# Optimization experiments

Measured on AMD Instinct MI355X. Metric: run time of the kernel, lower is better.

## Reference

```python
import jax, jax.numpy as jnp
import numpy as np

N_NODES = 50000
N_EDGES = 800000
HIDDEN = 128
N_LAYERS = 3
N_MASKED = 25000
N_GRAPHS = 64


def setup_inputs() -> dict:
    key = jax.random.key(0)
    ks = jax.random.split(key, 8)
    scale = 1.0 / np.sqrt(HIDDEN)
    return {
        "x": jax.random.normal(ks[0], (N_NODES, HIDDEN), dtype=jnp.float32),
        "edge_index": jax.random.randint(ks[1], (2, N_EDGES), 0, N_NODES, dtype=jnp.int64),
        "mask": jax.random.randint(ks[2], (N_MASKED,), 0, N_NODES, dtype=jnp.int64),
        "batch": jnp.sort(jax.random.randint(ks[3], (N_MASKED,), 0, N_GRAPHS, dtype=jnp.int64)),
        "conv_w": jax.random.normal(ks[4], (N_LAYERS, HIDDEN, HIDDEN), dtype=jnp.float32) * scale,
        "conv_b": jnp.zeros((N_LAYERS, HIDDEN), dtype=jnp.float32),
        "lt1_w": jax.random.normal(ks[5], (HIDDEN,), dtype=jnp.float32) * scale,
        "lt1_b": jnp.zeros((1,), dtype=jnp.float32),
    }


def reference(x, edge_index, mask, batch, conv_w, conv_b, lt1_w, lt1_b):
    n = x.shape[0]
    # GCNConv: add self-loops, symmetric normalization D^-1/2 (A+I) D^-1/2
    loops = jnp.arange(n, dtype=edge_index.dtype)
    src = jnp.concatenate([edge_index[0], loops])
    dst = jnp.concatenate([edge_index[1], loops])
    deg = jax.ops.segment_sum(jnp.ones_like(src, dtype=x.dtype), dst, num_segments=n)
    dinv = jax.lax.rsqrt(deg)  # deg >= 1 because of self-loops
    norm = (dinv[src] * dinv[dst])[:, None]  # [E+N, 1]

    h = x
    for l in range(N_LAYERS):
        hw = h @ conv_w[l]                                  # [N, H]
        agg = jax.ops.segment_sum(hw[src] * norm, dst, num_segments=n)
        h = jax.nn.elu(agg + conv_b[l])                     # dropout is identity in eval mode

    xm = h[mask]                                            # [M, H] masked-node features
    pooled = jax.ops.segment_max(xm, batch, num_segments=N_GRAPHS)  # global_max_pool
    return pooled @ lt1_w[:, None] + lt1_b                  # [G, 1]
```

## Files before the change

### kernel.cpp

```cpp
#include <hip/hip_runtime.h>
#include <math.h>

#define N_NODES  50000
#define N_EDGES  800000
#define HIDDEN   128
#define N_LAYERS 3
#define N_MASKED 25000
#define N_GRAPHS 64

typedef __attribute__((ext_vector_type(8))) short bf16x8;
typedef __attribute__((ext_vector_type(4))) float f32x4;

__device__ __forceinline__ unsigned fmap(float f) {
    unsigned u = __float_as_uint(f);
    return (u & 0x80000000u) ? ~u : (u | 0x80000000u);
}
__device__ __forceinline__ float funmap(unsigned u) {
    return __uint_as_float((u & 0x80000000u) ? (u & 0x7FFFFFFFu) : ~u);
}

__device__ __forceinline__ unsigned pack_split(float x) {
    unsigned u = __float_as_uint(x);
    unsigned hi = (u + 0x7fffu + ((u >> 16) & 1u)) >> 16;
    float rem = x - __uint_as_float(hi << 16);
    unsigned v = __float_as_uint(rem);
    unsigned lo = (v + 0x7fffu + ((v >> 16) & 1u)) >> 16;
    return hi | (lo << 16);
}

__global__ void count_deg_kernel(const int* __restrict__ dst, unsigned* __restrict__ deg) {
    int i = blockIdx.x * blockDim.x + threadIdx.x;
    if (i < N_EDGES) atomicAdd(&deg[dst[i]], 1u);
}

__global__ void dinv_kernel(const unsigned* __restrict__ deg, float* __restrict__ dinv) {
    int i = blockIdx.x * blockDim.x + threadIdx.x;
    if (i < N_NODES) dinv[i] = rsqrtf((float)(deg[i] + 1u));
}

__global__ void scan_block_kernel(const unsigned* __restrict__ deg, unsigned* __restrict__ incl,
                                  unsigned* __restrict__ bsum) {
    __shared__ unsigned s[1024];
    int i = blockIdx.x * 1024 + threadIdx.x;
    unsigned v = (i < N_NODES) ? deg[i] : 0u;
    s[threadIdx.x] = v;
    __syncthreads();
    for (int off = 1; off < 1024; off <<= 1) {
        unsigned t = (threadIdx.x >= off) ? s[threadIdx.x - off] : 0u;
        __syncthreads();
        s[threadIdx.x] += t;
        __syncthreads();
    }
    if (i < N_NODES) incl[i] = s[threadIdx.x];
    if (threadIdx.x == 1023) bsum[blockIdx.x] = s[1023];
}

__global__ void scan_bsum_kernel(unsigned* __restrict__ bsum, int n) {
    if (blockIdx.x == 0 && threadIdx.x == 0) {
        unsigned run = 0;
        for (int i = 0; i < n; ++i) { unsigned t = bsum[i]; bsum[i] = run; run += t; }
    }
}

__global__ void scan_finalize_kernel(const unsigned* __restrict__ incl,
                                     const unsigned* __restrict__ bsum_ex,
                                     unsigned* __restrict__ row_ptr,
                                     unsigned* __restrict__ cursor) {
    int i = blockIdx.x * blockDim.x + threadIdx.x;
    if (i <= N_NODES) {
        unsigned v = (i == 0) ? 0u : incl[i - 1] + bsum_ex[(i - 1) >> 10];
        row_ptr[i] = v;
        if (i < N_NODES) cursor[i] = v;
    }
}

__global__ void fill_csr_kernel(const int* __restrict__ src, const int* __restrict__ dst,
                                unsigned* __restrict__ cursor, int* __restrict__ csr_src) {
    int e = blockIdx.x * blockDim.x + threadIdx.x;
    if (e < N_EDGES) {
        unsigned p = atomicAdd(&cursor[dst[e]], 1u);
        csr_src[p] = src[e];
    }
}

__global__ void wprep_kernel(const float* __restrict__ W,
                             unsigned short* __restrict__ Whi,
                             unsigned short* __restrict__ Wlo) {
    int idx = blockIdx.x * 256 + threadIdx.x;
    if (idx >= 3 * 16384) return;
    int j     = idx & 7;
    int lane  = (idx >> 3) & 63;
    int ct    = (idx >> 9) & 7;
    int ks    = (idx >> 12) & 3;
    int layer = idx >> 14;
    int k = ks * 32 + (lane >> 4) * 8 + j;
    int n = ct * 16 + (lane & 15);
    unsigned p = pack_split(W[layer * 16384 + k * 128 + n]);
    Whi[idx] = (unsigned short)(p & 0xffffu);
    Wlo[idx] = (unsigned short)(p >> 16);
}

__global__ void xpack_kernel(const float* __restrict__ x, unsigned* __restrict__ xp, int n) {
    int i = blockIdx.x * 256 + threadIdx.x;
    if (i < n) xp[i] = pack_split(x[i]);
}

template<int MODE>
__global__ __launch_bounds__(256, 2) void mfma_gemm_kernel(const unsigned* __restrict__ Ap,
                                                           const unsigned short* __restrict__ Wh,
                                                           const unsigned short* __restrict__ Wl,
                                                           const float* __restrict__ dinv,
                                                           const float* __restrict__ bias,
                                                           const int* __restrict__ batch,
                                                           unsigned* __restrict__ gmax,
                                                           float* __restrict__ Out,
                                                           int nrows) {
    __shared__ __align__(16) unsigned short WhL[16384];
    __shared__ __align__(16) unsigned short WlL[16384];
    const int tid = threadIdx.x;
    const int lane = tid & 63;
    const int wv = tid >> 6;
    const int rowBase = blockIdx.x * 64 + wv * 16;
    const bool active = rowBase < nrows;

    int arow = rowBase + (lane & 15);
    if (arow > nrows - 1) arow = nrows - 1;
    const unsigned* aptr = Ap + (size_t)arow * 128 + (lane >> 4) * 8;
    uint4 pa[8];
    #pragma unroll
    for (int q = 0; q < 8; ++q)
        pa[q] = active ? *(const uint4*)(aptr + (q >> 1) * 32 + (q & 1) * 4)
                       : make_uint4(0, 0, 0, 0);

    {
        const uint4* gh = (const uint4*)Wh;
        const uint4* gl = (const uint4*)Wl;
        uint4* sh = (uint4*)WhL;
        uint4* sl = (uint4*)WlL;
        #pragma unroll
        for (int i = 0; i < 8; ++i) {
            sh[tid + i * 256] = gh[tid + i * 256];
            sl[tid + i * 256] = gl[tid + i * 256];
        }
    }
    __syncthreads();
    if (!active) return;

    f32x4 acc[8];
    #pragma unroll
    for (int c = 0; c < 8; ++c) acc[c] = (f32x4){0.f, 0.f, 0.f, 0.f};

    #pragma unroll
    for (int ks = 0; ks < 4; ++ks) {
        unsigned pv[8] = {pa[2*ks].x, pa[2*ks].y, pa[2*ks].z, pa[2*ks].w,
                          pa[2*ks+1].x, pa[2*ks+1].y, pa[2*ks+1].z, pa[2*ks+1].w};
        bf16x8 ah, al;
        #pragma unroll
        for (int j = 0; j < 8; ++j) {
            ah[j] = (short)(pv[j] & 0xffffu);
            al[j] = (short)(pv[j] >> 16);
        }
        const unsigned short* wbh = WhL + ks * 4096 + lane * 8;
        const unsigned short* wbl = WlL + ks * 4096 + lane * 8;
        #pragma unroll
        for (int ct = 0; ct < 8; ++ct) {
            bf16x8 bh = *(const bf16x8*)(wbh + ct * 512);
            bf16x8 bl = *(const bf16x8*)(wbl + ct * 512);
            acc[ct] = __builtin_amdgcn_mfma_f32_16x16x32_bf16(ah, bh, acc[ct], 0, 0, 0);
            acc[ct] = __builtin_amdgcn_mfma_f32_16x16x32_bf16(al, bh, acc[ct], 0, 0, 0);
            acc[ct] = __builtin_amdgcn_mfma_f32_16x16x32_bf16(ah, bl, acc[ct], 0, 0, 0);
        }
    }

    const int colBase = lane & 15;
    const int rgrp = lane >> 4;
    #pragma unroll
    for (int r = 0; r < 4; ++r) {
        int row = rowBase + rgrp * 4 + r;
        if (row >= nrows) continue;
        float d = 0.f;
        int bofs = 0;
        if (MODE == 0 || MODE == 1) d = dinv[row];
        if (MODE == 2) bofs = batch[row] * 128;
        #pragma unroll
        for (int ct = 0; ct < 8; ++ct) {
            int col = ct * 16 + colBase;
            float o = acc[ct][r];
            if (MODE == 0) {
                Out[(size_t)row * 128 + col] = o * d;
            } else {
                o += bias[col];
                o = o > 0.f ? o : expm1f(o);
                if (MODE == 1) Out[(size_t)row * 128 + col] = o * d;
                else           atomicMax(&gmax[bofs + col], fmap(o));
            }
        }
    }
}

template<int GMODE>
__global__ __launch_bounds__(256) void gather_kernel(const float* __restrict__ tab,
                                                     const unsigned* __restrict__ row_ptr,
                                                     const int* __restrict__ csr_src,
                                                     const float* __restrict__ dinv,
                                                     const float* __restrict__ bias,
                                                     float* __restrict__ outf,
                                                     unsigned* __restrict__ outp,
                                                     const int* __restrict__ nodes,
                                                     int n_items) {
    int wid = (blockIdx.x * blockDim.x + threadIdx.x) >> 6;
    int w = wid >> 1;
    if (w >= n_items) return;
    const int f = ((wid & 1) << 6) | (threadIdx.x & 63);
    const int v = nodes ? nodes[w] : w;

    const unsigned s0 = row_ptr[v], e0 = row_ptr[v + 1];
    const float* __restrict__ base = tab + f;

    float acc[8];
    #pragma unroll
    for (int j = 0; j < 8; ++j) acc[j] = 0.f;
    acc[0] = base[(size_t)v << 7];

    unsigned i = s0;
    if (i + 8 <= e0) {
        int idx[8];
        #pragma unroll
        for (int j = 0; j < 8; ++j) idx[j] = csr_src[i + j];
        for (; i + 16 <= e0; i += 8) {
            int nxt[8];
            #pragma unroll
            for (int j = 0; j < 8; ++j) nxt[j] = csr_src[i + 8 + j];
            #pragma unroll
            for (int j = 0; j < 8; ++j) acc[j] += base[(size_t)idx[j] << 7];
            #pragma unroll
            for (int j = 0; j < 8; ++j) idx[j] = nxt[j];
        }
        #pragma unroll
        for (int j = 0; j < 8; ++j) acc[j] += base[(size_t)idx[j] << 7];
        i += 8;
    }
    if (i + 4 <= e0) {
        #pragma unroll
        for (int j = 0; j < 4; ++j) acc[j] += base[(size_t)csr_src[i + j] << 7];
        i += 4;
    }
    for (; i < e0; ++i) acc[0] += base[(size_t)csr_src[i] << 7];

    float dv = dinv[v];
    float sumall = ((acc[0] + acc[1]) + (acc[2] + acc[3])) +
                   ((acc[4] + acc[5]) + (acc[6] + acc[7]));
    if (GMODE == 0) {
        float o = dv * sumall + bias[f];
        o = o > 0.f ? o : expm1f(o);
        outf[((size_t)w << 7) + f] = o * dv;
    } else {
        outp[((size_t)w << 7) + f] = pack_split(dv * sumall);
    }
}

__global__ void gmax_init_kernel(unsigned* __restrict__ gmax) {
    int i = blockIdx.x * blockDim.x + threadIdx.x;
    if (i < N_GRAPHS * 128) gmax[i] = 0x007FFFFFu;
}

__global__ void pool_finish_kernel(const unsigned* __restrict__ gmax,
                                   const float* __restrict__ w, const float* __restrict__ b,
                                   float* __restrict__ out) {
    const int g = blockIdx.x;
    const int f = threadIdx.x;
    float val = funmap(gmax[g * 128 + f]) * w[f];
    #pragma unroll
    for (int off = 32; off > 0; off >>= 1) val += __shfl_down(val, off);
    __shared__ float ps[2];
    if ((threadIdx.x & 63) == 0) ps[threadIdx.x >> 6] = val;
    __syncthreads();
    if (threadIdx.x == 0) out[g] = ps[0] + ps[1] + b[0];
}

extern "C" void kernel_launch(void* const* d_in, const int* in_sizes, int n_in,
                              void* d_out, int out_size, void* d_ws, size_t ws_size,
                              hipStream_t stream) {
    const float* x      = (const float*)d_in[0];
    const int*   ei     = (const int*)d_in[1];
    const int*   mask   = (const int*)d_in[2];
    const int*   batch  = (const int*)d_in[3];
    const float* conv_w = (const float*)d_in[4];
    const float* conv_b = (const float*)d_in[5];
    const float* lt1_w  = (const float*)d_in[6];
    const float* lt1_b  = (const float*)d_in[7];
    float* out = (float*)d_out;

    const int* e_src = ei;
    const int* e_dst = ei + N_EDGES;

    char* ws = (char*)d_ws;
    auto carve = [&](size_t bytes) { char* p = ws; ws += (bytes + 255) & ~(size_t)255; return p; };
    unsigned* deg     = (unsigned*)carve(N_NODES * 4);
    float*    dinv    = (float*)   carve(N_NODES * 4);
    unsigned* row_ptr = (unsigned*)carve((N_NODES + 1) * 4);
    unsigned* cursor  = (unsigned*)carve(N_NODES * 4);
    unsigned* bsum    = (unsigned*)carve(64 * 4);
    unsigned* gmax    = (unsigned*)carve(N_GRAPHS * 128 * 4);
    unsigned short* wph = (unsigned short*)carve(3 * 16384 * 2);
    unsigned short* wpl = (unsigned short*)carve(3 * 16384 * 2);
    int*      csr_src = (int*)     carve((size_t)N_EDGES * 4);
    char*     reg1    = carve((size_t)N_NODES * HIDDEN * 4);
    char*     reg2    = carve((size_t)N_NODES * HIDDEN * 4);
    unsigned* incl    = (unsigned*)csr_src;

    unsigned* xp    = (unsigned*)reg1;
    float*    bufB  = (float*)reg1;
    float*    bufB2 = (float*)reg1;
    float*    bufA  = (float*)reg2;
    unsigned* bufAp = (unsigned*)reg2;
    unsigned* bufCp = (unsigned*)reg2;

    const int NB_SCAN = (N_NODES + 1023) / 1024;

    hipMemsetAsync(deg, 0, N_NODES * sizeof(unsigned), stream);
    count_deg_kernel<<<(N_EDGES + 255) / 256, 256, 0, stream>>>(e_dst, deg);
    dinv_kernel<<<(N_NODES + 255) / 256, 256, 0, stream>>>(deg, dinv);
    scan_block_kernel<<<NB_SCAN, 1024, 0, stream>>>(deg, incl, bsum);
    scan_bsum_kernel<<<1, 64, 0, stream>>>(bsum, NB_SCAN);
    scan_finalize_kernel<<<(N_NODES + 256) / 256, 256, 0, stream>>>(incl, bsum, row_ptr, cursor);
    fill_csr_kernel<<<(N_EDGES + 255) / 256, 256, 0, stream>>>(e_src, e_dst, cursor, csr_src);
    gmax_init_kernel<<<(N_GRAPHS * 128 + 255) / 256, 256, 0, stream>>>(gmax);
    wprep_kernel<<<(3 * 16384 + 255) / 256, 256, 0, stream>>>(conv_w, wph, wpl);
    xpack_kernel<<<(N_NODES * HIDDEN + 255) / 256, 256, 0, stream>>>(x, xp, N_NODES * HIDDEN);

    const int GEMM_FULL = (N_NODES + 63) / 64;
    const int GEMM_MASK = (N_MASKED + 63) / 64;
    const int GA_FULL = (N_NODES * 2 * 64 + 255) / 256;
    const int GA_MASK = (N_MASKED * 2 * 64 + 255) / 256;

    mfma_gemm_kernel<0><<<GEMM_FULL, 256, 0, stream>>>(xp, wph, wpl, dinv, nullptr,
                                                       nullptr, nullptr, bufA, N_NODES);
    gather_kernel<0><<<GA_FULL, 256, 0, stream>>>(bufA, row_ptr, csr_src, dinv,
                                                  conv_b, bufB, nullptr, nullptr, N_NODES);
    gather_kernel<1><<<GA_FULL, 256, 0, stream>>>(bufB, row_ptr, csr_src, dinv,
                                                  nullptr, nullptr, bufAp, nullptr, N_NODES);
    mfma_gemm_kernel<1><<<GEMM_FULL, 256, 0, stream>>>(bufAp, wph + 16384, wpl + 16384, dinv,
                                                       conv_b + HIDDEN, nullptr, nullptr,
                                                       bufB2, N_NODES);
    gather_kernel<1><<<GA_MASK, 256, 0, stream>>>(bufB2, row_ptr, csr_src, dinv,
                                                  nullptr, nullptr, bufCp, mask, N_MASKED);
    mfma_gemm_kernel<2><<<GEMM_MASK, 256, 0, stream>>>(bufCp, wph + 32768, wpl + 32768, nullptr,
                                                       conv_b + 2 * HIDDEN, batch, gmax,
                                                       nullptr, N_MASKED);

    pool_finish_kernel<<<N_GRAPHS, HIDDEN, 0, stream>>>(gmax, lt1_w, lt1_b, out);
}
```

Before: 396.7 us.

## Store feature tables as 16-column slices and gather slice-wise with float4 lanes

The GEMM outputs and the layer-1 gather output now use a sliced layout: 8 slices of 16 columns, each slice stored contiguously for all nodes. The gather kernel assigns each block one slice and four nodes. Within a wave, 16 edges are processed in parallel with float4 loads of 64 bytes per row, and the partial sums are combined with shuffles. The goal is to keep each slice's working set (about 3.2 MB) resident in cache and to spread edge loads across lanes for more memory parallelism. In exchange, slice blocks repeat the index reads and row_ptr loads 8 times, and every gather ends with a shuffle reduction.

New measurement: 552.6 us. 39.3% more time.

```diff
diff --git a/kernel.cpp b/kernel.cpp
--- a/kernel.cpp
+++ b/kernel.cpp
@@ -7,6 +7,7 @@
 #define N_LAYERS 3
 #define N_MASKED 25000
 #define N_GRAPHS 64
+#define SLICE_STRIDE ((size_t)N_NODES * 16)
 
 typedef __attribute__((ext_vector_type(8))) short bf16x8;
 typedef __attribute__((ext_vector_type(4))) float f32x4;
@@ -113,7 +114,7 @@
                                                            const float* __restrict__ bias,
                                                            const int* __restrict__ batch,
                                                            unsigned* __restrict__ gmax,
-                                                           float* __restrict__ Out,
+                                                           float* __restrict__ OutS,
                                                            int nrows) {
     __shared__ __align__(16) unsigned short WhL[16384];
     __shared__ __align__(16) unsigned short WlL[16384];
@@ -187,75 +188,81 @@
             int col = ct * 16 + colBase;
             float o = acc[ct][r];
             if (MODE == 0) {
-                Out[(size_t)row * 128 + col] = o * d;
+                OutS[(size_t)ct * SLICE_STRIDE + (size_t)row * 16 + colBase] = o * d;
             } else {
                 o += bias[col];
                 o = o > 0.f ? o : expm1f(o);
-                if (MODE == 1) Out[(size_t)row * 128 + col] = o * d;
-                else           atomicMax(&gmax[bofs + col], fmap(o));
+                if (MODE == 1)
+                    OutS[(size_t)ct * SLICE_STRIDE + (size_t)row * 16 + colBase] = o * d;
+                else
+                    atomicMax(&gmax[bofs + col], fmap(o));
             }
         }
     }
 }
 
 template<int GMODE>
-__global__ __launch_bounds__(256) void gather_kernel(const float* __restrict__ tab,
+__global__ __launch_bounds__(256) void gather_kernel(const float* __restrict__ tabS,
                                                      const unsigned* __restrict__ row_ptr,
                                                      const int* __restrict__ csr_src,
                                                      const float* __restrict__ dinv,
                                                      const float* __restrict__ bias,
-                                                     float* __restrict__ outf,
+                                                     float* __restrict__ outS,
                                                      unsigned* __restrict__ outp,
                                                      const int* __restrict__ nodes,
                                                      int n_items) {
-    int wid = (blockIdx.x * blockDim.x + threadIdx.x) >> 6;
-    int w = wid >> 1;
+    const int b = blockIdx.x;
+    const int s = b & 7;
+    const int w = (b >> 3) * 4 + (threadIdx.x >> 6);
     if (w >= n_items) return;
-    const int f = ((wid & 1) << 6) | (threadIdx.x & 63);
+    const int lane = threadIdx.x & 63;
+    const int eq = lane >> 2;
+    const int q  = lane & 3;
     const int v = nodes ? nodes[w] : w;
 
+    const float4* __restrict__ tab4 = (const float4*)(tabS + (size_t)s * SLICE_STRIDE);
+
     const unsigned s0 = row_ptr[v], e0 = row_ptr[v + 1];
-    const float* __restrict__ base = tab + f;
-
-    float acc[8];
-    #pragma unroll
-    for (int j = 0; j < 8; ++j) acc[j] = 0.f;
-    acc[0] = base[(size_t)v << 7];
-
-    unsigned i = s0;
-    if (i + 8 <= e0) {
-        int idx[8];
-        #pragma unroll
-        for (int j = 0; j < 8; ++j) idx[j] = csr_src[i + j];
-        for (; i + 16 <= e0; i += 8) {
-            int nxt[8];
-            #pragma unroll
-            for (int j = 0; j < 8; ++j) nxt[j] = csr_src[i + 8 + j];
-            #pragma unroll
-            for (int j = 0; j < 8; ++j) acc[j] += base[(size_t)idx[j] << 7];
-            #pragma unroll
-            for (int j = 0; j < 8; ++j) idx[j] = nxt[j];
-        }
-        #pragma unroll
-        for (int j = 0; j < 8; ++j) acc[j] += base[(size_t)idx[j] << 7];
-        i += 8;
-    }
-    if (i + 4 <= e0) {
-        #pragma unroll
-        for (int j = 0; j < 4; ++j) acc[j] += base[(size_t)csr_src[i + j] << 7];
-        i += 4;
-    }
-    for (; i < e0; ++i) acc[0] += base[(size_t)csr_src[i] << 7];
-
-    float dv = dinv[v];
-    float sumall = ((acc[0] + acc[1]) + (acc[2] + acc[3])) +
-                   ((acc[4] + acc[5]) + (acc[6] + acc[7]));
-    if (GMODE == 0) {
-        float o = dv * sumall + bias[f];
-        o = o > 0.f ? o : expm1f(o);
-        outf[((size_t)w << 7) + f] = o * dv;
-    } else {
-        outp[((size_t)w << 7) + f] = pack_split(dv * sumall);
+    const int cnt = (int)(e0 - s0);
+
+    float4 a = make_float4(0.f, 0.f, 0.f, 0.f);
+    if (eq == 0) a = tab4[(size_t)v * 4 + q];
+
+    for (int i = 0; i < cnt; i += 16) {
+        int e = i + eq;
+        if (e < cnt) {
+            int src = csr_src[s0 + e];
+            float4 t = tab4[(size_t)src * 4 + q];
+            a.x += t.x; a.y += t.y; a.z += t.z; a.w += t.w;
+        }
+    }
+
+    #pragma unroll
+    for (int off = 32; off >= 4; off >>= 1) {
+        a.x += __shfl_down(a.x, off);
+        a.y += __shfl_down(a.y, off);
+        a.z += __shfl_down(a.z, off);
+        a.w += __shfl_down(a.w, off);
+    }
+
+    if (lane < 4) {
+        float dv = dinv[v];
+        if (GMODE == 0) {
+            float4 bb = *(const float4*)&bias[s * 16 + lane * 4];
+            float4 o;
+            o.x = dv * a.x + bb.x; o.y = dv * a.y + bb.y;
+            o.z = dv * a.z + bb.z; o.w = dv * a.w + bb.w;
+            o.x = o.x > 0.f ? o.x : expm1f(o.x);
+            o.y = o.y > 0.f ? o.y : expm1f(o.y);
+            o.z = o.z > 0.f ? o.z : expm1f(o.z);
+            o.w = o.w > 0.f ? o.w : expm1f(o.w);
+            o.x *= dv; o.y *= dv; o.z *= dv; o.w *= dv;
+            ((float4*)(outS + (size_t)s * SLICE_STRIDE + (size_t)w * 16))[lane] = o;
+        } else {
+            uint4 pk = make_uint4(pack_split(dv * a.x), pack_split(dv * a.y),
+                                  pack_split(dv * a.z), pack_split(dv * a.w));
+            ((uint4*)(outp + (size_t)w * 128 + s * 16))[lane] = pk;
+        }
     }
 }
 
@@ -331,20 +338,20 @@
 
     const int GEMM_FULL = (N_NODES + 63) / 64;
     const int GEMM_MASK = (N_MASKED + 63) / 64;
-    const int GA_FULL = (N_NODES * 2 * 64 + 255) / 256;
-    const int GA_MASK = (N_MASKED * 2 * 64 + 255) / 256;
+    const int GA_FULL_BLK = 8 * ((N_NODES + 3) / 4);
+    const int GA_MASK_BLK = 8 * ((N_MASKED + 3) / 4);
 
     mfma_gemm_kernel<0><<<GEMM_FULL, 256, 0, stream>>>(xp, wph, wpl, dinv, nullptr,
                                                        nullptr, nullptr, bufA, N_NODES);
-    gather_kernel<0><<<GA_FULL, 256, 0, stream>>>(bufA, row_ptr, csr_src, dinv,
-                                                  conv_b, bufB, nullptr, nullptr, N_NODES);
-    gather_kernel<1><<<GA_FULL, 256, 0, stream>>>(bufB, row_ptr, csr_src, dinv,
-                                                  nullptr, nullptr, bufAp, nullptr, N_NODES);
+    gather_kernel<0><<<GA_FULL_BLK, 256, 0, stream>>>(bufA, row_ptr, csr_src, dinv,
+                                                      conv_b, bufB, nullptr, nullptr, N_NODES);
+    gather_kernel<1><<<GA_FULL_BLK, 256, 0, stream>>>(bufB, row_ptr, csr_src, dinv,
+                                                      nullptr, nullptr, bufAp, nullptr, N_NODES);
     mfma_gemm_kernel<1><<<GEMM_FULL, 256, 0, stream>>>(bufAp, wph + 16384, wpl + 16384, dinv,
                                                        conv_b + HIDDEN, nullptr, nullptr,
                                                        bufB2, N_NODES);
-    gather_kernel<1><<<GA_MASK, 256, 0, stream>>>(bufB2, row_ptr, csr_src, dinv,
-                                                  nullptr, nullptr, bufCp, mask, N_MASKED);
+    gather_kernel<1><<<GA_MASK_BLK, 256, 0, stream>>>(bufB2, row_ptr, csr_src, dinv,
+                                                      nullptr, nullptr, bufCp, mask, N_MASKED);
     mfma_gemm_kernel<2><<<GEMM_MASK, 256, 0, stream>>>(bufCp, wph + 32768, wpl + 32768, nullptr,
                                                        conv_b + 2 * HIDDEN, batch, gmax,
                                                        nullptr, N_MASKED);
```
